# Kernel tuning notes

Hardware: AMD Instinct MI355X
Metric: run time of the kernel (lower is better)

Reference implementation:

```python
import jax, jax.numpy as jnp
import numpy as np

N, E, G = 50000, 640000, 128
IN_DIM, LAT, H, HID, NC = 128, 32, 8, 128, 2


def setup_inputs() -> dict:
    key = jax.random.key(0)
    ks = jax.random.split(key, 16)
    x = jax.random.normal(ks[0], (N, IN_DIM), dtype=jnp.float32)
    edge_index = jax.random.randint(ks[1], (2, E), 0, N, dtype=jnp.int64)
    # contiguous graph blocks covering all G graph ids
    batch = (jnp.arange(N, dtype=jnp.int64) * G) // N
    y = jax.random.randint(ks[2], (G,), 0, NC, dtype=jnp.int64)

    def lin(k, fi, fo):
        return jax.random.normal(k, (fi, fo), dtype=jnp.float32) / np.sqrt(fi)

    return {
        'x': x, 'edge_index': edge_index, 'batch': batch, 'y': y,
        'W1': lin(ks[3], IN_DIM, LAT), 'b1': jnp.zeros((LAT,), jnp.float32),
        'Wg1': lin(ks[4], LAT, H * LAT),
        'asrc1': jax.random.normal(ks[5], (H, LAT), jnp.float32) / np.sqrt(LAT),
        'adst1': jax.random.normal(ks[6], (H, LAT), jnp.float32) / np.sqrt(LAT),
        'bg1': jnp.zeros((H * LAT,), jnp.float32),
        'Wg2': lin(ks[7], H * LAT, H * LAT),
        'asrc2': jax.random.normal(ks[8], (H, LAT), jnp.float32) / np.sqrt(LAT),
        'adst2': jax.random.normal(ks[9], (H, LAT), jnp.float32) / np.sqrt(LAT),
        'bg2': jnp.zeros((H * LAT,), jnp.float32),
        'Wl1': lin(ks[10], LAT + 2 * H * LAT, HID), 'bl1': jnp.zeros((HID,), jnp.float32),
        'Wl2': lin(ks[11], HID, NC), 'bl2': jnp.zeros((NC,), jnp.float32),
    }


def _add_self_loops(edge_index, n):
    loop = jnp.arange(n, dtype=edge_index.dtype)
    row = jnp.concatenate([edge_index[0], loop])
    col = jnp.concatenate([edge_index[1], loop])
    return row, col


def gcn_conv(x, row, col, W, b):
    h = x @ W  # [N, C]
    deg = jax.ops.segment_sum(jnp.ones_like(col, dtype=h.dtype), col, num_segments=N)
    dinv = jax.lax.rsqrt(jnp.maximum(deg, 1.0))  # self-loops guarantee deg >= 1
    norm = dinv[row] * dinv[col]  # [E']
    return jax.ops.segment_sum(norm[:, None] * h[row], col, num_segments=N) + b


def gat_conv(x, row, col, W, a_src, a_dst, b):
    h = (x @ W).reshape(N, H, LAT)  # [N, H, C]
    s = jnp.einsum('nhc,hc->nh', h, a_src)
    d = jnp.einsum('nhc,hc->nh', h, a_dst)
    logits = jax.nn.leaky_relu(s[row] + d[col], negative_slope=0.2)  # [E', H]
    m = jax.ops.segment_max(logits, col, num_segments=N)
    m = jnp.where(jnp.isfinite(m), m, 0.0)
    e = jnp.exp(logits - m[col])
    z = jax.ops.segment_sum(e, col, num_segments=N)
    alpha = e / (z[col] + 1e-16)  # segment softmax over incoming edges
    out = jax.ops.segment_sum(alpha[:, :, None] * h[row], col, num_segments=N)
    return out.reshape(N, H * LAT) + b


def reference(x, edge_index, batch, y, W1, b1, Wg1, asrc1, adst1, bg1,
              Wg2, asrc2, adst2, bg2, Wl1, bl1, Wl2, bl2):
    row, col = _add_self_loops(edge_index, N)
    h1 = jax.nn.elu(gcn_conv(x, row, col, W1, b1))
    h2 = jax.nn.elu(gat_conv(h1, row, col, Wg1, asrc1, adst1, bg1))
    h3 = jax.nn.elu(gat_conv(h2, row, col, Wg2, asrc2, adst2, bg2))
    cat = jnp.concatenate([h1, h2, h3], axis=1)  # [N, 544]
    # first node of each graph (batch is sorted, contiguous blocks)
    idx = jnp.searchsorted(batch, jnp.arange(G, dtype=batch.dtype))
    feature = cat[idx] @ Wl1 + bl1  # [G, HID]
    hidden = jax.nn.elu(feature)  # eval mode: dropout off
    raw = hidden @ Wl2 + bl2
    prob = jax.nn.softmax(raw, axis=1)
    logits = jax.nn.log_softmax(raw, axis=1)
    loss = -jnp.mean(jnp.take_along_axis(logits, y[:, None], axis=1))
    pred = jnp.argmax(logits, axis=1, keepdims=True)
    return logits, loss, pred, prob, feature
```

## Files before the change

### kernel.cpp

```cpp
#include <hip/hip_runtime.h>
#include <math.h>

#define NN 50000
#define EE 640000
#define EP (EE + NN)
#define GG 128
#define IND 128
#define LATC 32
#define HH 8
#define HLC 256
#define HIDN 128
#define SCAN_B 256
#define SCAN_G ((NN + SCAN_B - 1) / SCAN_B)
#define AGP_BLOCKS 2048

typedef unsigned short ushortT;
typedef unsigned int uintT;
typedef short bf16x8 __attribute__((ext_vector_type(8)));
typedef float f32x4 __attribute__((ext_vector_type(4)));

__device__ __forceinline__ float elu1(float v) { return v > 0.f ? v : (__expf(v) - 1.f); }

__device__ __forceinline__ ushortT f2bf(float f) {
  unsigned int u = __float_as_uint(f);
  return (ushortT)((u + 0x7fffu + ((u >> 16) & 1u)) >> 16);
}
__device__ __forceinline__ float bf2f(ushortT s) {
  return __uint_as_float(((unsigned int)s) << 16);
}

__global__ void count_kernel(const int* col, int* cnt) {
  int t = blockIdx.x * blockDim.x + threadIdx.x;
  if (t < EE) atomicAdd(&cnt[col[t]], 1);
}

__global__ void scan_part_kernel(const int* __restrict__ cnt,
                                 int* __restrict__ bsum) {
  int t = threadIdx.x;
  int i = blockIdx.x * SCAN_B + t;
  int v = (i < NN) ? cnt[i] + 1 : 0;
#pragma unroll
  for (int d = 1; d < 64; d <<= 1) v += __shfl_xor(v, d);
  __shared__ int ws[4];
  if ((t & 63) == 0) ws[t >> 6] = v;
  __syncthreads();
  if (t == 0) bsum[blockIdx.x] = ws[0] + ws[1] + ws[2] + ws[3];
}

__global__ void scan_top_kernel(const int* __restrict__ bsum,
                                int* __restrict__ ebsum,
                                int* __restrict__ offs_last) {
  int t = threadIdx.x;
  int v = (t < SCAN_G) ? bsum[t] : 0;
  int orig = v;
  int lane = t & 63, w = t >> 6;
#pragma unroll
  for (int d = 1; d < 64; d <<= 1) {
    int o = __shfl_up(v, d);
    if (lane >= d) v += o;
  }
  __shared__ int ws[4];
  if (lane == 63) ws[w] = v;
  __syncthreads();
  int add = 0;
  for (int j = 0; j < w; ++j) add += ws[j];
  v += add;
  if (t < SCAN_G) ebsum[t] = v - orig;
  if (t == SCAN_G - 1) *offs_last = v;
}

__global__ void scan_final_kernel(const int* __restrict__ cnt,
                                  const int* __restrict__ ebsum,
                                  int* __restrict__ offs,
                                  float* __restrict__ dinv) {
  int t = threadIdx.x;
  int i = blockIdx.x * SCAN_B + t;
  int v = (i < NN) ? cnt[i] + 1 : 0;
  int orig = v;
  int lane = t & 63, w = t >> 6;
#pragma unroll
  for (int d = 1; d < 64; d <<= 1) {
    int o = __shfl_up(v, d);
    if (lane >= d) v += o;
  }
  __shared__ int ws[4];
  if (lane == 63) ws[w] = v;
  __syncthreads();
  int add = ebsum[blockIdx.x];
  for (int j = 0; j < w; ++j) add += ws[j];
  if (i < NN) {
    offs[i] = v - orig + add;
    dinv[i] = 1.f / sqrtf((float)orig);
  }
}

__global__ void build_kernel(const int* row, const int* col, const int* offs,
                             int* cursor, int* srcs) {
  int t = blockIdx.x * blockDim.x + threadIdx.x;
  if (t >= EP) return;
  int r, c;
  if (t < EE) { r = row[t]; c = col[t]; } else { r = t - EE; c = r; }
  int pos = offs[c] + atomicAdd(&cursor[c], 1);
  srcs[pos] = r;
}

__global__ void finalize_kernel(const int* offs, int* srcs) {
  int gw = (blockIdx.x * blockDim.x + threadIdx.x) >> 6;
  if (gw >= NN) return;
  int lane = threadIdx.x & 63;
  int beg = offs[gw], end = offs[gw + 1];
  int deg = end - beg;
  if (deg <= 64) {
    int v = (lane < deg) ? srcs[beg + lane] : 0x7fffffff;
    for (int k = 2; k <= 64; k <<= 1)
      for (int j = k >> 1; j > 0; j >>= 1) {
        int o = __shfl_xor(v, j);
        bool keepmin = (((lane & k) == 0) == ((lane & j) == 0));
        v = keepmin ? (v < o ? v : o) : (v > o ? v : o);
      }
    if (lane < deg) srcs[beg + lane] = v;
  } else if (lane == 0) {
    for (int i = beg + 1; i < end; ++i) {
      int v = srcs[i]; int j = i - 1;
      while (j >= beg && srcs[j] > v) { srcs[j + 1] = srcs[j]; --j; }
      srcs[j + 1] = v;
    }
  }
}

__global__ void prep_kernel(const float* __restrict__ Wg1,
                            const float* __restrict__ asrc,
                            const float* __restrict__ adst, float* va,
                            float* vb) {
  int t = threadIdx.x;
  int c = t & 31, h = t >> 5;
  float sa = 0.f, sb = 0.f;
  for (int j = 0; j < 32; ++j) {
    float w = Wg1[(size_t)c * HLC + h * 32 + j];
    sa += w * asrc[h * 32 + j];
    sb += w * adst[h * 32 + j];
  }
  va[t] = sa;
  vb[t] = sb;
}

__launch_bounds__(256)
__global__ void gemm_in_kernel(const float* __restrict__ A,
                               const float* __restrict__ W,
                               float* __restrict__ out) {
  __shared__ float As[32][264];
  __shared__ float Bs[32][32];
  int bm = blockIdx.x * 256;
  int tid = threadIdx.x;
  int tx = tid & 7, ty = tid >> 3;
  float acc[8][4] = {};
  for (int k0 = 0; k0 < IND; k0 += 32) {
    {
      int gm = bm + tid;
      bool ok = gm < NN;
#pragma unroll
      for (int j = 0; j < 8; ++j) {
        float4 v = ok ? *(const float4*)(A + (size_t)gm * IND + k0 + j * 4)
                      : make_float4(0.f, 0.f, 0.f, 0.f);
        As[j * 4 + 0][tid] = v.x; As[j * 4 + 1][tid] = v.y;
        As[j * 4 + 2][tid] = v.z; As[j * 4 + 3][tid] = v.w;
      }
    }
#pragma unroll
    for (int j = 0; j < 4; ++j) {
      int idx = tid + j * 256;
      int kk = idx >> 5, c = idx & 31;
      Bs[kk][c] = W[(size_t)(k0 + kk) * LATC + c];
    }
    __syncthreads();
#pragma unroll 4
    for (int kk = 0; kk < 32; ++kk) {
      float4 a0 = *(const float4*)(&As[kk][ty * 8]);
      float4 a1 = *(const float4*)(&As[kk][ty * 8 + 4]);
      float4 b = *(const float4*)(&Bs[kk][tx * 4]);
      float ar[8] = {a0.x, a0.y, a0.z, a0.w, a1.x, a1.y, a1.z, a1.w};
      float bc[4] = {b.x, b.y, b.z, b.w};
#pragma unroll
      for (int i = 0; i < 8; ++i)
#pragma unroll
        for (int j = 0; j < 4; ++j) acc[i][j] += ar[i] * bc[j];
    }
    __syncthreads();
  }
#pragma unroll
  for (int i = 0; i < 8; ++i) {
    int gm = bm + ty * 8 + i;
    if (gm < NN)
      *(float4*)(out + (size_t)gm * LATC + tx * 4) =
          make_float4(acc[i][0], acc[i][1], acc[i][2], acc[i][3]);
  }
}

__global__ void wsplit_kernel(const float* __restrict__ Wg2,
                              ushortT* __restrict__ WhT,
                              ushortT* __restrict__ WlT) {
  int idx = blockIdx.x * 256 + threadIdx.x;
  if (idx >= HLC * HLC) return;
  int k = idx >> 8, n = idx & 255;
  float f = Wg2[idx];
  ushortT hi = f2bf(f);
  WhT[n * HLC + k] = hi;
  WlT[n * HLC + k] = f2bf(f - bf2f(hi));
}

__launch_bounds__(256)
__global__ void gemm_gat2_mfma(const float* __restrict__ A,
                               const ushortT* __restrict__ WhT,
                               const ushortT* __restrict__ WlT,
                               const float* __restrict__ asrc,
                               const float* __restrict__ adst,
                               ushortT* __restrict__ hgb,
                               float* __restrict__ sbuf,
                               float* __restrict__ dbuf) {
  __shared__ __align__(16) char smem[51200];
  ushortT* Ah = (ushortT*)smem;
  ushortT* Al = Ah + 64 * 40;
  ushortT* Bh = (ushortT*)(smem + 10240);
  ushortT* Bl = Bh + 256 * 40;
  float* LDSf = (float*)(smem + 10240);

  int tid = threadIdx.x;
  int lane = tid & 63;
  int w = tid >> 6;
  int l15 = lane & 15, lg = lane >> 4;
  int bm = blockIdx.x * 64;

  f32x4 zero4 = {0.f, 0.f, 0.f, 0.f};
  f32x4 acc[4][4];
#pragma unroll
  for (int mi = 0; mi < 4; ++mi)
#pragma unroll
    for (int ni = 0; ni < 4; ++ni) acc[mi][ni] = zero4;

  for (int k0 = 0; k0 < HLC; k0 += 32) {
    {
      int row = tid >> 2, kb = (tid & 3) * 8;
      int gm = bm + row;
      float f[8];
      if (gm < NN) {
        float4 u0 = *(const float4*)(A + (size_t)gm * HLC + k0 + kb);
        float4 u1 = *(const float4*)(A + (size_t)gm * HLC + k0 + kb + 4);
        f[0] = u0.x; f[1] = u0.y; f[2] = u0.z; f[3] = u0.w;
        f[4] = u1.x; f[5] = u1.y; f[6] = u1.z; f[7] = u1.w;
      } else {
#pragma unroll
        for (int j = 0; j < 8; ++j) f[j] = 0.f;
      }
      bf16x8 vh, vl;
#pragma unroll
      for (int j = 0; j < 8; ++j) {
        ushortT hi = f2bf(f[j]);
        vh[j] = (short)hi;
        vl[j] = (short)f2bf(f[j] - bf2f(hi));
      }
      *(bf16x8*)(Ah + row * 40 + kb) = vh;
      *(bf16x8*)(Al + row * 40 + kb) = vl;
    }
    {
      const bf16x8* ph = (const bf16x8*)(WhT + (size_t)tid * HLC + k0);
      const bf16x8* pl = (const bf16x8*)(WlT + (size_t)tid * HLC + k0);
#pragma unroll
      for (int i = 0; i < 4; ++i) {
        *(bf16x8*)(Bh + tid * 40 + i * 8) = ph[i];
        *(bf16x8*)(Bl + tid * 40 + i * 8) = pl[i];
      }
    }
    __syncthreads();
    bf16x8 ah[4], al[4], bh[4], bl[4];
#pragma unroll
    for (int mi = 0; mi < 4; ++mi) {
      int off = (mi * 16 + l15) * 40 + lg * 8;
      ah[mi] = *(const bf16x8*)(Ah + off);
      al[mi] = *(const bf16x8*)(Al + off);
    }
#pragma unroll
    for (int ni = 0; ni < 4; ++ni) {
      int off = (w * 64 + ni * 16 + l15) * 40 + lg * 8;
      bh[ni] = *(const bf16x8*)(Bh + off);
      bl[ni] = *(const bf16x8*)(Bl + off);
    }
#pragma unroll
    for (int mi = 0; mi < 4; ++mi)
#pragma unroll
      for (int ni = 0; ni < 4; ++ni) {
        acc[mi][ni] = __builtin_amdgcn_mfma_f32_16x16x32_bf16(
            al[mi], bh[ni], acc[mi][ni], 0, 0, 0);
        acc[mi][ni] = __builtin_amdgcn_mfma_f32_16x16x32_bf16(
            ah[mi], bl[ni], acc[mi][ni], 0, 0, 0);
        acc[mi][ni] = __builtin_amdgcn_mfma_f32_16x16x32_bf16(
            ah[mi], bh[ni], acc[mi][ni], 0, 0, 0);
      }
    __syncthreads();
  }

  float av[4], bv[4];
#pragma unroll
  for (int ni = 0; ni < 4; ++ni) {
    int c = w * 64 + ni * 16 + l15;
    av[ni] = asrc[c];
    bv[ni] = adst[c];
  }
#pragma unroll
  for (int mi = 0; mi < 4; ++mi)
#pragma unroll
    for (int r = 0; r < 4; ++r) {
      int gm = bm + mi * 16 + lg * 4 + r;
      float s0 = acc[mi][0][r] * av[0] + acc[mi][1][r] * av[1];
      float s1 = acc[mi][2][r] * av[2] + acc[mi][3][r] * av[3];
      float d0 = acc[mi][0][r] * bv[0] + acc[mi][1][r] * bv[1];
      float d1 = acc[mi][2][r] * bv[2] + acc[mi][3][r] * bv[3];
#pragma unroll
      for (int m = 1; m <= 8; m <<= 1) {
        s0 += __shfl_xor(s0, m);
        s1 += __shfl_xor(s1, m);
        d0 += __shfl_xor(d0, m);
        d1 += __shfl_xor(d1, m);
      }
      if (l15 == 0 && gm < NN) {
        sbuf[gm * HH + 2 * w] = s0;
        sbuf[gm * HH + 2 * w + 1] = s1;
        dbuf[gm * HH + 2 * w] = d0;
        dbuf[gm * HH + 2 * w + 1] = d1;
      }
    }

#pragma unroll
  for (int p = 0; p < 2; ++p) {
    __syncthreads();
#pragma unroll
    for (int q = 0; q < 2; ++q) {
      int mi = 2 * p + q;
#pragma unroll
      for (int ni = 0; ni < 4; ++ni)
#pragma unroll
        for (int r = 0; r < 4; ++r) {
          int lrow = q * 16 + lg * 4 + r;
          LDSf[lrow * 260 + w * 64 + ni * 16 + l15] = acc[mi][ni][r];
        }
    }
    __syncthreads();
    int row = tid >> 3, cb = (tid & 7) * 32;
    int gm = bm + p * 32 + row;
    if (gm < NN) {
      uintT u[16];
#pragma unroll
      for (int i = 0; i < 8; ++i) {
        float4 v = *(const float4*)(LDSf + row * 260 + cb + i * 4);
        u[2 * i] = (uintT)f2bf(v.x) | ((uintT)f2bf(v.y) << 16);
        u[2 * i + 1] = (uintT)f2bf(v.z) | ((uintT)f2bf(v.w) << 16);
      }
      uintT* dst = (uintT*)(hgb + (size_t)gm * HLC + cb);
#pragma unroll
      for (int i = 0; i < 4; ++i) {
        uint4 s;
        s.x = u[4 * i]; s.y = u[4 * i + 1];
        s.z = u[4 * i + 2]; s.w = u[4 * i + 3];
        *(uint4*)(dst + 4 * i) = s;
      }
    }
  }
}

__global__ void gcn_agg_sd_kernel(const float* __restrict__ hW,
                                  const int* offs, const int* srcs,
                                  const float* dinv, const float* b1,
                                  const float* __restrict__ vag,
                                  const float* __restrict__ vbg,
                                  float* h1, float* s, float* d) {
  __shared__ float va[HLC], vb[HLC];
  __shared__ float rowbuf[4][LATC];
  int t = threadIdx.x;
  va[t] = vag[t];
  vb[t] = vbg[t];
  __syncthreads();
  int wid = (blockIdx.x * blockDim.x + t) >> 6;
  int lane = t & 63;
  int wv = t >> 6;
  int c = lane & 31, half = lane >> 5;
  int beg = offs[wid], end = offs[wid + 1];
  float acc = 0.f;
  for (int p = beg + half; p < end; p += 2) {
    int src = srcs[p];
    acc += dinv[src] * hW[src * LATC + c];
  }
  acc += __shfl_xor(acc, 32);
  if (lane < 32) {
    float v = elu1(dinv[wid] * acc + b1[c]);
    h1[wid * LATC + c] = v;
    rowbuf[wv][c] = v;
  }
  int h = lane >> 3, k = lane & 7;
  float ps = 0.f, pd = 0.f;
#pragma unroll
  for (int j = 0; j < 4; ++j) {
    float x = rowbuf[wv][k * 4 + j];
    ps += x * va[h * 32 + k * 4 + j];
    pd += x * vb[h * 32 + k * 4 + j];
  }
  ps += __shfl_xor(ps, 1); pd += __shfl_xor(pd, 1);
  ps += __shfl_xor(ps, 2); pd += __shfl_xor(pd, 2);
  ps += __shfl_xor(ps, 4); pd += __shfl_xor(pd, 4);
  if (k == 0) {
    s[wid * HH + h] = ps;
    d[wid * HH + h] = pd;
  }
}

__launch_bounds__(256)
__global__ void gat1_aggproj_kernel(const float* __restrict__ h1,
                                    const float* __restrict__ s,
                                    const float* __restrict__ d,
                                    const int* offs, const int* srcs,
                                    const float* __restrict__ Wg1,
                                    const float* __restrict__ bg,
                                    float* __restrict__ h2) {
  __shared__ float Ws[32][HLC];
  __shared__ float aggs[4][HLC];
  int t = threadIdx.x;
  {
    const float4* Wv = (const float4*)Wg1;
    float4* Bv = (float4*)Ws;
#pragma unroll
    for (int i = 0; i < 8; ++i) Bv[t + i * 256] = Wv[t + i * 256];
  }
  __syncthreads();
  int lane = t & 63;
  int wv = t >> 6;
  int g = lane >> 5, l5 = lane & 31;
  int h = l5 >> 2, c8 = (l5 & 3) * 8;
  int qb = lane * 4, hq = lane >> 3;
  float4 bb = *(const float4*)(bg + qb);
  for (int wid = blockIdx.x * 4 + wv; wid < NN; wid += AGP_BLOCKS * 4) {
    int beg = offs[wid], end = offs[wid + 1];
    float dn = d[wid * HH + h];
    float self = s[wid * HH + h] + dn;
    float m = self > 0.f ? self : 0.2f * self;
    float z = 0.f;
    float a[8] = {};
#pragma unroll 2
    for (int p = beg + g; p < end; p += 2) {
      int src = srcs[p];
      float sv = s[src * HH + h] + dn;
      float logit = sv > 0.f ? sv : 0.2f * sv;
      float e = __expf(logit - m);
      z += e;
      float4 v0 = *(const float4*)(h1 + (size_t)src * LATC + c8);
      float4 v1 = *(const float4*)(h1 + (size_t)src * LATC + c8 + 4);
      a[0] += e * v0.x; a[1] += e * v0.y; a[2] += e * v0.z; a[3] += e * v0.w;
      a[4] += e * v1.x; a[5] += e * v1.y; a[6] += e * v1.z; a[7] += e * v1.w;
    }
    z += __shfl_xor(z, 32);
#pragma unroll
    for (int j = 0; j < 8; ++j) a[j] += __shfl_xor(a[j], 32);
    float zinv = 1.f / (z + 1e-16f);
    if (g == 0) {
#pragma unroll
      for (int j = 0; j < 8; ++j)
        aggs[wv][h * 32 + c8 + j] = a[j] * zinv;
    }
    float o0 = bb.x, o1 = bb.y, o2 = bb.z, o3 = bb.w;
#pragma unroll 8
    for (int cc = 0; cc < 32; ++cc) {
      float av = aggs[wv][hq * 32 + cc];
      float4 w4 = *(const float4*)(&Ws[cc][qb]);
      o0 += av * w4.x; o1 += av * w4.y; o2 += av * w4.z; o3 += av * w4.w;
    }
    *(float4*)(h2 + (size_t)wid * HLC + qb) =
        make_float4(elu1(o0), elu1(o1), elu1(o2), elu1(o3));
  }
}

__global__ void gat_agg_kernel(const ushortT* __restrict__ hgb,
                               const float* __restrict__ s,
                               const float* __restrict__ dd, const int* offs,
                               const int* srcs, const float* bg, float* out) {
  int wid = (blockIdx.x * blockDim.x + threadIdx.x) >> 6;
  if (wid >= NN) return;
  int lane = threadIdx.x & 63;
  int hh = lane >> 3;
  int ch = lane << 2;
  int beg = offs[wid], end = offs[wid + 1];
  float dn = dd[wid * HH + hh];
  float self = s[wid * HH + hh] + dn;
  float m = self > 0.f ? self : 0.2f * self;
  float z = 0.f;
  float ax = 0.f, ay = 0.f, az = 0.f, aw = 0.f;
#pragma unroll 4
  for (int p = beg; p < end; ++p) {
    int src = srcs[p];
    float xv = s[src * HH + hh] + dn;
    float logit = xv > 0.f ? xv : 0.2f * xv;
    float e = __expf(logit - m);
    z += e;
    ushort4 v = *(const ushort4*)(hgb + (size_t)src * HLC + ch);
    ax += e * bf2f(v.x); ay += e * bf2f(v.y);
    az += e * bf2f(v.z); aw += e * bf2f(v.w);
  }
  float zinv = 1.f / (z + 1e-16f);
  float4 bb = *(const float4*)(bg + ch);
  float4 o;
  o.x = elu1(ax * zinv + bb.x); o.y = elu1(ay * zinv + bb.y);
  o.z = elu1(az * zinv + bb.z); o.w = elu1(aw * zinv + bb.w);
  *(float4*)(out + (size_t)wid * HLC + ch) = o;
}

__global__ void head_kernel(const float* __restrict__ h1,
                            const float* __restrict__ h2,
                            const float* __restrict__ h3, const int* batch,
                            const int* y, const float* __restrict__ Wl1,
                            const float* bl1, const float* __restrict__ Wl2,
                            const float* bl2, float* out, float* lterms,
                            int* done) {
  int g = blockIdx.x, tid = threadIdx.x;
  __shared__ float cat[544];
  __shared__ float hidden[HIDN];
  __shared__ float raw_s[2];
  __shared__ int idx_s;
  if (tid == 0) {
    int lo = 0, hi = NN;
    while (lo < hi) { int mid = (lo + hi) >> 1; if (batch[mid] < g) lo = mid + 1; else hi = mid; }
    idx_s = lo;
  }
  __syncthreads();
  int idx = idx_s;
  if (tid < 32) cat[tid] = h1[idx * LATC + tid];
  for (int i = tid; i < HLC; i += HIDN) {
    cat[32 + i] = h2[(size_t)idx * HLC + i];
    cat[288 + i] = h3[(size_t)idx * HLC + i];
  }
  __syncthreads();
  float f = bl1[tid];
  for (int k = 0; k < 544; ++k) f += cat[k] * Wl1[k * HIDN + tid];
  out[641 + g * HIDN + tid] = f;
  hidden[tid] = elu1(f);
  __syncthreads();
  if (tid < 2) {
    float r = bl2[tid];
    for (int j = 0; j < HIDN; ++j) r += hidden[j] * Wl2[j * 2 + tid];
    raw_s[tid] = r;
  }
  __syncthreads();
  if (tid == 0) {
    float r0 = raw_s[0], r1 = raw_s[1];
    float mx = fmaxf(r0, r1);
    float e0 = expf(r0 - mx), e1 = expf(r1 - mx);
    float zz = e0 + e1;
    float lse = mx + logf(zz);
    float lg0 = r0 - lse, lg1 = r1 - lse;
    out[g * 2 + 0] = lg0; out[g * 2 + 1] = lg1;
    out[385 + g * 2 + 0] = e0 / zz; out[385 + g * 2 + 1] = e1 / zz;
    out[257 + g] = (r1 > r0) ? 1.f : 0.f;
    lterms[g] = -((y[g] == 0) ? lg0 : lg1);
    __threadfence();
    int ticket = atomicAdd(done, 1);
    if (ticket == GG - 1) {
      __threadfence();
      float sum = 0.f;
      for (int j = 0; j < GG; ++j) sum += lterms[j];
      out[256] = sum / (float)GG;
    }
  }
}

extern "C" void kernel_launch(void* const* d_in, const int* in_sizes, int n_in,
                              void* d_out, int out_size, void* d_ws,
                              size_t ws_size, hipStream_t stream) {
  const float* x = (const float*)d_in[0];
  const int* ei = (const int*)d_in[1];
  const int* batch = (const int*)d_in[2];
  const int* y = (const int*)d_in[3];
  const float* W1 = (const float*)d_in[4];
  const float* b1 = (const float*)d_in[5];
  const float* Wg1 = (const float*)d_in[6];
  const float* asrc1 = (const float*)d_in[7];
  const float* adst1 = (const float*)d_in[8];
  const float* bg1 = (const float*)d_in[9];
  const float* Wg2 = (const float*)d_in[10];
  const float* asrc2 = (const float*)d_in[11];
  const float* adst2 = (const float*)d_in[12];
  const float* bg2 = (const float*)d_in[13];
  const float* Wl1 = (const float*)d_in[14];
  const float* bl1 = (const float*)d_in[15];
  const float* Wl2 = (const float*)d_in[16];
  const float* bl2 = (const float*)d_in[17];
  float* out = (float*)d_out;

  const int* erow = ei;
  const int* ecol = ei + EE;

  char* p = (char*)d_ws;
  auto alloc = [&](size_t bytes) {
    void* r = (void*)p;
    p += (bytes + 255) & ~(size_t)255;
    return r;
  };
  int* cntcur = (int*)alloc(((size_t)2 * NN + 64) * 4);
  int* cnt = cntcur;
  int* cursor = cntcur + NN;
  int* done = cntcur + 2 * NN;
  int* offs = (int*)alloc((NN + 1) * 4);
  int* srcs = (int*)alloc((size_t)EP * 4);
  int* bsum = (int*)alloc(SCAN_G * 4);
  int* ebsum = (int*)alloc(SCAN_G * 4);
  float* dinv = (float*)alloc(NN * 4);
  float* hW = (float*)alloc((size_t)NN * LATC * 4);
  float* h1 = (float*)alloc((size_t)NN * LATC * 4);
  float* hg = (float*)alloc((size_t)NN * HLC * 4);
  float* h2 = (float*)alloc((size_t)NN * HLC * 4);
  float* h3 = (float*)alloc((size_t)NN * HLC * 4);
  float* sbuf = (float*)alloc((size_t)NN * HH * 4);
  float* dbuf = (float*)alloc((size_t)NN * HH * 4);
  float* va = (float*)alloc(HLC * 4);
  float* vb = (float*)alloc(HLC * 4);
  float* lterms = (float*)alloc(GG * 4);
  ushortT* whT = (ushortT*)alloc((size_t)HLC * HLC * 2);
  ushortT* wlT = (ushortT*)alloc((size_t)HLC * HLC * 2);
  ushortT* hgb = (ushortT*)hg;

  const int NBLK = (NN + 63) / 64;

  hipMemsetAsync(cntcur, 0, ((size_t)2 * NN + 64) * 4, stream);
  count_kernel<<<(EE + 255) / 256, 256, 0, stream>>>(ecol, cnt);
  scan_part_kernel<<<SCAN_G, SCAN_B, 0, stream>>>(cnt, bsum);
  scan_top_kernel<<<1, 256, 0, stream>>>(bsum, ebsum, offs + NN);
  scan_final_kernel<<<SCAN_G, SCAN_B, 0, stream>>>(cnt, ebsum, offs, dinv);
  build_kernel<<<(EP + 255) / 256, 256, 0, stream>>>(erow, ecol, offs, cursor, srcs);
  finalize_kernel<<<(NN + 3) / 4, 256, 0, stream>>>(offs, srcs);

  wsplit_kernel<<<(HLC * HLC + 255) / 256, 256, 0, stream>>>(Wg2, whT, wlT);
  prep_kernel<<<1, 256, 0, stream>>>(Wg1, asrc1, adst1, va, vb);

  gemm_in_kernel<<<(NN + 255) / 256, 256, 0, stream>>>(x, W1, hW);
  gcn_agg_sd_kernel<<<(NN + 3) / 4, 256, 0, stream>>>(
      hW, offs, srcs, dinv, b1, va, vb, h1, sbuf, dbuf);

  gat1_aggproj_kernel<<<AGP_BLOCKS, 256, 0, stream>>>(h1, sbuf, dbuf, offs,
                                                      srcs, Wg1, bg1, h2);

  gemm_gat2_mfma<<<NBLK, 256, 0, stream>>>(h2, whT, wlT, asrc2, adst2, hgb,
                                           sbuf, dbuf);
  gat_agg_kernel<<<(NN + 3) / 4, 256, 0, stream>>>(hgb, sbuf, dbuf, offs, srcs, bg2, h3);

  head_kernel<<<GG, HIDN, 0, stream>>>(h1, h2, h3, batch, y, Wl1, bl1, Wl2,
                                       bl2, out, lterms, done);
}
```

Baseline: 360.2 us.

## Split fused GAT1 aggregation+projection into separate agg and tiled GEMM kernels

Replaces the persistent fused kernel, which aggregated each node's neighbours and then projected through Wg1 held in shared memory, with two kernels. The first is a one-wave-per-node attention aggregation that writes the normalized per-head aggregates to a global buffer. The second is a register-tiled block-diagonal GEMM that applies Wg1, bias and ELU over 32-node tiles. The aim is to free the gather kernel from the large shared-memory footprint and serialized per-node projection, which should raise occupancy and compute efficiency. In exchange it adds a full N×256 float intermediate that must be written and read back, plus an extra launch.

```diff
diff --git a/kernel.cpp b/kernel.cpp
--- a/kernel.cpp
+++ b/kernel.cpp
@@ -12,7 +12,6 @@
 #define HIDN 128
 #define SCAN_B 256
 #define SCAN_G ((NN + SCAN_B - 1) / SCAN_B)
-#define AGP_BLOCKS 2048
 
 typedef unsigned short ushortT;
 typedef unsigned int uintT;
@@ -411,16 +410,55 @@
   }
 }
 
+__global__ void gat1_agg_kernel(const float* __restrict__ h1,
+                                const float* __restrict__ s,
+                                const float* __restrict__ dd, const int* offs,
+                                const int* srcs, float* __restrict__ agg) {
+  int wid = (blockIdx.x * blockDim.x + threadIdx.x) >> 6;
+  if (wid >= NN) return;
+  int lane = threadIdx.x & 63;
+  int g = lane >> 5;
+  int l5 = lane & 31;
+  int h = l5 >> 2;
+  int c8 = (l5 & 3) * 8;
+  int beg = offs[wid], end = offs[wid + 1];
+  float dn = dd[wid * HH + h];
+  float self = s[wid * HH + h] + dn;
+  float m = self > 0.f ? self : 0.2f * self;
+  float z = 0.f;
+  float a[8] = {};
+#pragma unroll 2
+  for (int p = beg + g; p < end; p += 2) {
+    int src = srcs[p];
+    float sv = s[src * HH + h] + dn;
+    float logit = sv > 0.f ? sv : 0.2f * sv;
+    float e = __expf(logit - m);
+    z += e;
+    float4 v0 = *(const float4*)(h1 + (size_t)src * LATC + c8);
+    float4 v1 = *(const float4*)(h1 + (size_t)src * LATC + c8 + 4);
+    a[0] += e * v0.x; a[1] += e * v0.y; a[2] += e * v0.z; a[3] += e * v0.w;
+    a[4] += e * v1.x; a[5] += e * v1.y; a[6] += e * v1.z; a[7] += e * v1.w;
+  }
+  z += __shfl_xor(z, 32);
+#pragma unroll
+  for (int j = 0; j < 8; ++j) a[j] += __shfl_xor(a[j], 32);
+  if (g == 0) {
+    float zinv = 1.f / (z + 1e-16f);
+    *(float4*)(agg + (size_t)wid * HLC + h * LATC + c8) =
+        make_float4(a[0] * zinv, a[1] * zinv, a[2] * zinv, a[3] * zinv);
+    *(float4*)(agg + (size_t)wid * HLC + h * LATC + c8 + 4) =
+        make_float4(a[4] * zinv, a[5] * zinv, a[6] * zinv, a[7] * zinv);
+  }
+}
+
 __launch_bounds__(256)
-__global__ void gat1_aggproj_kernel(const float* __restrict__ h1,
-                                    const float* __restrict__ s,
-                                    const float* __restrict__ d,
-                                    const int* offs, const int* srcs,
-                                    const float* __restrict__ Wg1,
-                                    const float* __restrict__ bg,
-                                    float* __restrict__ h2) {
+__global__ void gat1_proj_kernel(const float* __restrict__ agg,
+                                 const float* __restrict__ Wg1,
+                                 const float* __restrict__ bg,
+                                 float* __restrict__ h2) {
+  __shared__ float As[HLC][32];
   __shared__ float Ws[32][HLC];
-  __shared__ float aggs[4][HLC];
+  int bm = blockIdx.x * 32;
   int t = threadIdx.x;
   {
     const float4* Wv = (const float4*)Wg1;
@@ -428,50 +466,57 @@
 #pragma unroll
     for (int i = 0; i < 8; ++i) Bv[t + i * 256] = Wv[t + i * 256];
   }
-  __syncthreads();
-  int lane = t & 63;
-  int wv = t >> 6;
-  int g = lane >> 5, l5 = lane & 31;
-  int h = l5 >> 2, c8 = (l5 & 3) * 8;
-  int qb = lane * 4, hq = lane >> 3;
-  float4 bb = *(const float4*)(bg + qb);
-  for (int wid = blockIdx.x * 4 + wv; wid < NN; wid += AGP_BLOCKS * 4) {
-    int beg = offs[wid], end = offs[wid + 1];
-    float dn = d[wid * HH + h];
-    float self = s[wid * HH + h] + dn;
-    float m = self > 0.f ? self : 0.2f * self;
-    float z = 0.f;
-    float a[8] = {};
-#pragma unroll 2
-    for (int p = beg + g; p < end; p += 2) {
-      int src = srcs[p];
-      float sv = s[src * HH + h] + dn;
-      float logit = sv > 0.f ? sv : 0.2f * sv;
-      float e = __expf(logit - m);
-      z += e;
-      float4 v0 = *(const float4*)(h1 + (size_t)src * LATC + c8);
-      float4 v1 = *(const float4*)(h1 + (size_t)src * LATC + c8 + 4);
-      a[0] += e * v0.x; a[1] += e * v0.y; a[2] += e * v0.z; a[3] += e * v0.w;
-      a[4] += e * v1.x; a[5] += e * v1.y; a[6] += e * v1.z; a[7] += e * v1.w;
-    }
-    z += __shfl_xor(z, 32);
-#pragma unroll
-    for (int j = 0; j < 8; ++j) a[j] += __shfl_xor(a[j], 32);
-    float zinv = 1.f / (z + 1e-16f);
-    if (g == 0) {
-#pragma unroll
-      for (int j = 0; j < 8; ++j)
-        aggs[wv][h * 32 + c8 + j] = a[j] * zinv;
-    }
-    float o0 = bb.x, o1 = bb.y, o2 = bb.z, o3 = bb.w;
-#pragma unroll 8
-    for (int cc = 0; cc < 32; ++cc) {
-      float av = aggs[wv][hq * 32 + cc];
-      float4 w4 = *(const float4*)(&Ws[cc][qb]);
-      o0 += av * w4.x; o1 += av * w4.y; o2 += av * w4.z; o3 += av * w4.w;
-    }
-    *(float4*)(h2 + (size_t)wid * HLC + qb) =
-        make_float4(elu1(o0), elu1(o1), elu1(o2), elu1(o3));
+  {
+    int n = t & 31, cb = (t >> 5) * 32;
+    int gm = bm + n;
+#pragma unroll
+    for (int j = 0; j < 8; ++j) {
+      float4 v = make_float4(0.f, 0.f, 0.f, 0.f);
+      if (gm < NN) v = *(const float4*)(agg + (size_t)gm * HLC + cb + j * 4);
+      As[cb + j * 4 + 0][n] = v.x;
+      As[cb + j * 4 + 1][n] = v.y;
+      As[cb + j * 4 + 2][n] = v.z;
+      As[cb + j * 4 + 3][n] = v.w;
+    }
+  }
+  __syncthreads();
+  int tx = t & 31, ty = t >> 5;
+  int h1o = (tx >> 3) * 32;
+  int h2o = 128 + (tx >> 3) * 32;
+  float acc1[4][4] = {}, acc2[4][4] = {};
+#pragma unroll 4
+  for (int kk = 0; kk < 32; ++kk) {
+    float4 a1 = *(const float4*)(&As[h1o + kk][ty * 4]);
+    float4 a2 = *(const float4*)(&As[h2o + kk][ty * 4]);
+    float4 w1 = *(const float4*)(&Ws[kk][tx * 4]);
+    float4 w2 = *(const float4*)(&Ws[kk][128 + tx * 4]);
+    float ar1[4] = {a1.x, a1.y, a1.z, a1.w};
+    float ar2[4] = {a2.x, a2.y, a2.z, a2.w};
+    float wr1[4] = {w1.x, w1.y, w1.z, w1.w};
+    float wr2[4] = {w2.x, w2.y, w2.z, w2.w};
+#pragma unroll
+    for (int r = 0; r < 4; ++r)
+#pragma unroll
+      for (int q = 0; q < 4; ++q) {
+        acc1[r][q] += ar1[r] * wr1[q];
+        acc2[r][q] += ar2[r] * wr2[q];
+      }
+  }
+  float4 b1 = *(const float4*)(bg + tx * 4);
+  float4 b2 = *(const float4*)(bg + 128 + tx * 4);
+  float bb1[4] = {b1.x, b1.y, b1.z, b1.w};
+  float bb2[4] = {b2.x, b2.y, b2.z, b2.w};
+#pragma unroll
+  for (int r = 0; r < 4; ++r) {
+    int gm = bm + ty * 4 + r;
+    if (gm >= NN) continue;
+    float4 o1, o2;
+    o1.x = elu1(acc1[r][0] + bb1[0]); o1.y = elu1(acc1[r][1] + bb1[1]);
+    o1.z = elu1(acc1[r][2] + bb1[2]); o1.w = elu1(acc1[r][3] + bb1[3]);
+    o2.x = elu1(acc2[r][0] + bb2[0]); o2.y = elu1(acc2[r][1] + bb2[1]);
+    o2.z = elu1(acc2[r][2] + bb2[2]); o2.w = elu1(acc2[r][3] + bb2[3]);
+    *(float4*)(h2 + (size_t)gm * HLC + tx * 4) = o1;
+    *(float4*)(h2 + (size_t)gm * HLC + 128 + tx * 4) = o2;
   }
 }
 
@@ -639,8 +684,8 @@
   gcn_agg_sd_kernel<<<(NN + 3) / 4, 256, 0, stream>>>(
       hW, offs, srcs, dinv, b1, va, vb, h1, sbuf, dbuf);
 
-  gat1_aggproj_kernel<<<AGP_BLOCKS, 256, 0, stream>>>(h1, sbuf, dbuf, offs,
-                                                      srcs, Wg1, bg1, h2);
+  gat1_agg_kernel<<<(NN + 3) / 4, 256, 0, stream>>>(h1, sbuf, dbuf, offs, srcs, hg);
+  gat1_proj_kernel<<<(NN + 31) / 32, 256, 0, stream>>>(hg, Wg1, bg1, h2);
 
   gemm_gat2_mfma<<<NBLK, 256, 0, stream>>>(h2, whT, wlT, asrc2, adst2, hgb,
                                            sbuf, dbuf);
```

Result: slower. 370.8 us (+2.9%).

## Keep GAT1 projection weights in registers and share projection across block

Applied to the files above, without the earlier changes.

The fused GAT layer-1 aggregate-and-project kernel no longer stages the 32x256 weight matrix in shared memory. Each thread keeps one weight column in registers and computes one output channel for each of the block's four nodes, reading the aggregated vectors from a padded shared buffer. This removes the per-block shared-memory weight load and the float4 LDS weight reads in the projection. In exchange it adds two block-wide barriers per iteration, so the four wavefronts, whose nodes have different degrees, must wait for each other, and it raises register pressure.

```diff
diff --git a/kernel.cpp b/kernel.cpp
--- a/kernel.cpp
+++ b/kernel.cpp
@@ -419,59 +419,60 @@
                                     const float* __restrict__ Wg1,
                                     const float* __restrict__ bg,
                                     float* __restrict__ h2) {
-  __shared__ float Ws[32][HLC];
-  __shared__ float aggs[4][HLC];
+  __shared__ float aggs[4][264];
   int t = threadIdx.x;
-  {
-    const float4* Wv = (const float4*)Wg1;
-    float4* Bv = (float4*)Ws;
-#pragma unroll
-    for (int i = 0; i < 8; ++i) Bv[t + i * 256] = Wv[t + i * 256];
-  }
-  __syncthreads();
+  float Wcol[32];
+#pragma unroll
+  for (int c = 0; c < 32; ++c) Wcol[c] = Wg1[(size_t)c * HLC + t];
+  float bias = bg[t];
+  int hp = t >> 5;
   int lane = t & 63;
   int wv = t >> 6;
   int g = lane >> 5, l5 = lane & 31;
   int h = l5 >> 2, c8 = (l5 & 3) * 8;
-  int qb = lane * 4, hq = lane >> 3;
-  float4 bb = *(const float4*)(bg + qb);
-  for (int wid = blockIdx.x * 4 + wv; wid < NN; wid += AGP_BLOCKS * 4) {
-    int beg = offs[wid], end = offs[wid + 1];
-    float dn = d[wid * HH + h];
-    float self = s[wid * HH + h] + dn;
-    float m = self > 0.f ? self : 0.2f * self;
-    float z = 0.f;
-    float a[8] = {};
+  for (int big = blockIdx.x * 4; big < NN; big += AGP_BLOCKS * 4) {
+    int wid = big + wv;
+    if (wid < NN) {
+      int beg = offs[wid], end = offs[wid + 1];
+      float dn = d[wid * HH + h];
+      float self = s[wid * HH + h] + dn;
+      float m = self > 0.f ? self : 0.2f * self;
+      float z = 0.f;
+      float a[8] = {};
 #pragma unroll 2
-    for (int p = beg + g; p < end; p += 2) {
-      int src = srcs[p];
-      float sv = s[src * HH + h] + dn;
-      float logit = sv > 0.f ? sv : 0.2f * sv;
-      float e = __expf(logit - m);
-      z += e;
-      float4 v0 = *(const float4*)(h1 + (size_t)src * LATC + c8);
-      float4 v1 = *(const float4*)(h1 + (size_t)src * LATC + c8 + 4);
-      a[0] += e * v0.x; a[1] += e * v0.y; a[2] += e * v0.z; a[3] += e * v0.w;
-      a[4] += e * v1.x; a[5] += e * v1.y; a[6] += e * v1.z; a[7] += e * v1.w;
-    }
-    z += __shfl_xor(z, 32);
-#pragma unroll
-    for (int j = 0; j < 8; ++j) a[j] += __shfl_xor(a[j], 32);
-    float zinv = 1.f / (z + 1e-16f);
-    if (g == 0) {
-#pragma unroll
-      for (int j = 0; j < 8; ++j)
-        aggs[wv][h * 32 + c8 + j] = a[j] * zinv;
-    }
-    float o0 = bb.x, o1 = bb.y, o2 = bb.z, o3 = bb.w;
-#pragma unroll 8
-    for (int cc = 0; cc < 32; ++cc) {
-      float av = aggs[wv][hq * 32 + cc];
-      float4 w4 = *(const float4*)(&Ws[cc][qb]);
-      o0 += av * w4.x; o1 += av * w4.y; o2 += av * w4.z; o3 += av * w4.w;
-    }
-    *(float4*)(h2 + (size_t)wid * HLC + qb) =
-        make_float4(elu1(o0), elu1(o1), elu1(o2), elu1(o3));
+      for (int p = beg + g; p < end; p += 2) {
+        int src = srcs[p];
+        float sv = s[src * HH + h] + dn;
+        float logit = sv > 0.f ? sv : 0.2f * sv;
+        float e = __expf(logit - m);
+        z += e;
+        float4 v0 = *(const float4*)(h1 + (size_t)src * LATC + c8);
+        float4 v1 = *(const float4*)(h1 + (size_t)src * LATC + c8 + 4);
+        a[0] += e * v0.x; a[1] += e * v0.y; a[2] += e * v0.z; a[3] += e * v0.w;
+        a[4] += e * v1.x; a[5] += e * v1.y; a[6] += e * v1.z; a[7] += e * v1.w;
+      }
+      z += __shfl_xor(z, 32);
+#pragma unroll
+      for (int j = 0; j < 8; ++j) a[j] += __shfl_xor(a[j], 32);
+      if (g == 0) {
+        float zinv = 1.f / (z + 1e-16f);
+#pragma unroll
+        for (int j = 0; j < 8; ++j)
+          aggs[wv][h * 33 + c8 + j] = a[j] * zinv;
+      }
+    }
+    __syncthreads();
+#pragma unroll
+    for (int n = 0; n < 4; ++n) {
+      int nd = big + n;
+      if (nd < NN) {
+        float o = bias;
+#pragma unroll
+        for (int c = 0; c < 32; ++c) o += aggs[n][hp * 33 + c] * Wcol[c];
+        h2[(size_t)nd * HLC + t] = elu1(o);
+      }
+    }
+    __syncthreads();
   }
 }
 
```

Result: slower. 373.7 us (+3.7%).
